# Kernel optimization log

Measured on AMD Instinct MI355X. Metric: run time of the kernel, lower is better.

Reference implementation:

```python
import jax, jax.numpy as jnp
import numpy as np

N, S, IN_F, TEXT_D, EMB, H = 128, 1024, 768, 512, 512, 8
HD = EMB // H  # 64


def setup_inputs() -> dict:
    key = jax.random.key(0)
    ks = jax.random.split(key, 14)
    sc = 0.02
    return {
        "v": jax.random.normal(ks[0], (1, N, 12, IN_F), dtype=jnp.float32),
        "t": jax.random.normal(ks[1], (N, S, TEXT_D), dtype=jnp.float32),
        "t_len": jax.random.randint(ks[2], (N,), 1, S + 1, dtype=jnp.int32),
        "W_fc1": jax.random.normal(ks[3], (EMB, IN_F), dtype=jnp.float32) * sc,
        "b_fc1": jnp.zeros((EMB,), jnp.float32),
        "W_fc2": jax.random.normal(ks[4], (EMB, 12 * EMB), dtype=jnp.float32) * sc,
        "b_fc2": jnp.zeros((EMB,), jnp.float32),
        "Wq": jax.random.normal(ks[5], (EMB, EMB), dtype=jnp.float32) * sc,
        "Wk": jax.random.normal(ks[6], (EMB, TEXT_D), dtype=jnp.float32) * sc,
        "Wv": jax.random.normal(ks[7], (EMB, TEXT_D), dtype=jnp.float32) * sc,
        "bq": jnp.zeros((EMB,), jnp.float32),
        "bk": jnp.zeros((EMB,), jnp.float32),
        "bv": jnp.zeros((EMB,), jnp.float32),
        "Wo": jax.random.normal(ks[8], (EMB, EMB), dtype=jnp.float32) * sc,
        "bo": jnp.zeros((EMB,), jnp.float32),
    }


def reference(v, t, t_len, W_fc1, b_fc1, W_fc2, b_fc2, Wq, Wk, Wv, bq, bk, bv, Wo, bo):
    # fc1 + ReLU: [1,N,12,IN_F] -> [N,12,EMB]
    x = jax.nn.relu(jnp.einsum('onif,ef->onie', v, W_fc1) + b_fc1)[0]
    # flatten + fc2 + ReLU -> [N, EMB]
    x = x.reshape(N, 12 * EMB)
    vfeat = jax.nn.relu(x @ W_fc2.T + b_fc2)
    # Batched ragged multihead attention, query length 1 per item.
    scale = 1.0 / jnp.sqrt(jnp.asarray(HD, vfeat.dtype))
    q = ((vfeat @ Wq.T + bq) * scale).reshape(N, H, HD)           # [N,H,HD]
    k = (jnp.einsum('nsd,ed->nse', t, Wk) + bk).reshape(N, S, H, HD)
    vv = (jnp.einsum('nsd,ed->nse', t, Wv) + bv).reshape(N, S, H, HD)
    scores = jnp.einsum('nhd,nshd->nhs', q, k)                    # [N,H,S]
    valid = (jnp.arange(S)[None, :] < t_len[:, None])[:, None, :]  # [N,1,S]
    scores = jnp.where(valid, scores, jnp.finfo(scores.dtype).min)
    w = jax.nn.softmax(scores, axis=-1)                           # [N,H,S]
    ctx = jnp.einsum('nhs,nshd->nhd', w, vv).reshape(N, EMB)
    attn_out = ctx @ Wo.T + bo                                    # [N,EMB]
    return vfeat, attn_out
```

## Files before the change

### kernel.cpp

```cpp
#include <hip/hip_runtime.h>

#define NB 128
#define SSEQ 1024
#define TD 512
#define NSPLIT 16

typedef _Float16 half8 __attribute__((ext_vector_type(8)));
typedef _Float16 half4 __attribute__((ext_vector_type(4)));
typedef _Float16 half2v __attribute__((ext_vector_type(2)));
typedef float f32x4 __attribute__((ext_vector_type(4)));
typedef float f32x2 __attribute__((ext_vector_type(2)));

__global__ __launch_bounds__(256) void k_cvt(
    const float* __restrict__ v, const float* __restrict__ w1,
    const float* __restrict__ w2, const float* __restrict__ wq,
    const float* __restrict__ wv, const float* __restrict__ wo,
    _Float16* __restrict__ v16, _Float16* __restrict__ w1h,
    _Float16* __restrict__ w2h, _Float16* __restrict__ wqh,
    _Float16* __restrict__ wvh, _Float16* __restrict__ woh)
{
  int i = blockIdx.x * 256 + threadIdx.x;
  const float* src; _Float16* dst; long j;
  if      (i < 294912)  { src = v;  dst = v16; j = i; }
  else if (i < 393216)  { src = w1; dst = w1h; j = i - 294912; }
  else if (i < 1179648) { src = w2; dst = w2h; j = i - 393216; }
  else if (i < 1245184) { src = wq; dst = wqh; j = i - 1179648; }
  else if (i < 1310720) { src = wv; dst = wvh; j = i - 1245184; }
  else if (i < 1376256) { src = wo; dst = woh; j = i - 1310720; }
  else return;
  f32x4 x = *(const f32x4*)(src + 4 * j);
  *(half4*)(dst + 4 * j) = __builtin_convertvector(x, half4);
}

__global__ __launch_bounds__(256) void k_gemm(
    const _Float16* __restrict__ A, int lda, long aSZ,
    const _Float16* __restrict__ B, int ldb, long bSZ,
    const float* __restrict__ bias, float scale, int doRelu, int outMode,
    float* __restrict__ outF, _Float16* __restrict__ outH,
    int ldc, int cColOff, int mtiles, int kTiles, long oSplit)
{
  __shared__ _Float16 As[64][72];
  __shared__ _Float16 Bs[64][72];
  int mt = blockIdx.x % mtiles, nt = blockIdx.x / mtiles;
  int sp = blockIdx.y, bz = blockIdx.z;
  int tid = threadIdx.x;
  int r = tid >> 2, kq = (tid & 3) * 16;
  int w = tid >> 6, l = tid & 63;
  const _Float16* Ab = A + (long)bz * aSZ + (long)(mt * 64) * lda + (long)sp * kTiles * 64;
  const _Float16* Bb = B + (long)bz * bSZ + (long)(nt * 64) * ldb + (long)sp * kTiles * 64;
  const _Float16* ap = Ab + (long)r * lda + kq;
  const _Float16* bp = Bb + (long)r * ldb + kq;
  half8 ag0 = *(const half8*)ap, ag1 = *(const half8*)(ap + 8);
  half8 bg0 = *(const half8*)bp, bg1 = *(const half8*)(bp + 8);
  f32x4 acc[4];
  #pragma unroll
  for (int c = 0; c < 4; ++c) acc[c] = (f32x4){0.f, 0.f, 0.f, 0.f};
  int fr = l & 15, fo = (l >> 4) * 8;
  for (int kt = 0; kt < kTiles; ++kt) {
    __syncthreads();
    *(half8*)&As[r][kq] = ag0; *(half8*)&As[r][kq + 8] = ag1;
    *(half8*)&Bs[r][kq] = bg0; *(half8*)&Bs[r][kq + 8] = bg1;
    __syncthreads();
    if (kt + 1 < kTiles) {
      ap += 64; bp += 64;
      ag0 = *(const half8*)ap; ag1 = *(const half8*)(ap + 8);
      bg0 = *(const half8*)bp; bg1 = *(const half8*)(bp + 8);
    }
    #pragma unroll
    for (int ks = 0; ks < 2; ++ks) {
      half8 af = *(const half8*)&As[16 * w + fr][ks * 32 + fo];
      #pragma unroll
      for (int c = 0; c < 4; ++c) {
        half8 bf = *(const half8*)&Bs[16 * c + fr][ks * 32 + fo];
        acc[c] = __builtin_amdgcn_mfma_f32_16x16x32_f16(af, bf, acc[c], 0, 0, 0);
      }
    }
  }
  int lrow = (l >> 4) * 4, lcol = l & 15;
  #pragma unroll
  for (int c = 0; c < 4; ++c) {
    #pragma unroll
    for (int rr = 0; rr < 4; ++rr) {
      int gm = mt * 64 + 16 * w + lrow + rr;
      int gn = nt * 64 + 16 * c + lcol;
      int ecol = gn + bz * cColOff;
      float vv = acc[c][rr];
      if (bias) vv += bias[ecol];
      vv *= scale;
      if (doRelu) vv = fmaxf(vv, 0.f);
      long oidx = (long)gm * ldc + ecol;
      if (outMode == 0) outF[oidx] = vv;
      else if (outMode == 1) outH[oidx] = (_Float16)vv;
      else outF[oidx + (long)sp * oSplit] = vv;
    }
  }
}

__global__ __launch_bounds__(256) void k_vfeat(
    const float* __restrict__ vacc, const float* __restrict__ b2,
    float* __restrict__ outF, _Float16* __restrict__ vf16)
{
  int i = blockIdx.x * 256 + threadIdx.x;
  float vv = b2[i & 511];
  #pragma unroll
  for (int sp = 0; sp < 16; ++sp) vv += vacc[sp * 65536 + i];
  vv = fmaxf(vv, 0.f);
  outF[i] = vv;
  vf16[i] = (_Float16)vv;
}

__global__ __launch_bounds__(256) void k_qk(
    const float* __restrict__ qacc, const float* __restrict__ bq,
    const float* __restrict__ Wk, const float* __restrict__ bk,
    _Float16* __restrict__ qk16, float* __restrict__ qb)
{
  int n = blockIdx.x, tid = threadIdx.x;
  __shared__ float qs[512];
  #pragma unroll
  for (int o = 0; o < 2; ++o) {
    int d = tid + o * 256;
    float q0 = qacc[n * 512 + d] + qacc[65536 + n * 512 + d]
             + qacc[131072 + n * 512 + d] + qacc[196608 + n * 512 + d];
    qs[d] = (q0 + bq[d]) * 0.125f;
  }
  __syncthreads();
  _Float16* qn = qk16 + (long)n * 8192;
  #pragma unroll 1
  for (int h = 0; h < 8; ++h) {
    float a0 = 0.f, a1 = 0.f;
    #pragma unroll 8
    for (int j = 0; j < 64; ++j) {
      float qv = qs[h * 64 + j];
      const float* wr = Wk + (long)(h * 64 + j) * 512;
      a0 = fmaf(qv, wr[tid], a0);
      a1 = fmaf(qv, wr[tid + 256], a1);
    }
    qn[h * 512 + tid] = (_Float16)a0;
    qn[h * 512 + tid + 256] = (_Float16)a1;
  }
  #pragma unroll
  for (int h = 8; h < 16; ++h) {
    qn[h * 512 + tid] = (_Float16)0.f;
    qn[h * 512 + tid + 256] = (_Float16)0.f;
  }
  if (tid < 64) {
    #pragma unroll 1
    for (int h = 0; h < 8; ++h) {
      float pb = qs[h * 64 + tid] * bk[h * 64 + tid];
      #pragma unroll
      for (int m = 1; m < 64; m <<= 1) pb += __shfl_xor(pb, m, 64);
      if (tid == 0) qb[n * 8 + h] = pb;
    }
  }
}

__global__ __launch_bounds__(256, 4) void k_attn(
    const float* __restrict__ t, const int* __restrict__ tlen,
    const _Float16* __restrict__ qk16, const float* __restrict__ qb,
    float* __restrict__ pu, float* __restrict__ pl)
{
  int n = blockIdx.x >> 4, sp = blockIdx.x & 15;
  int len = tlen[n];
  int chunk = (len + NSPLIT - 1) / NSPLIT;
  int s0 = sp * chunk;
  int s1 = s0 + chunk; if (s1 > len) s1 = len;
  if (s0 >= s1) return;
  int tid = threadIdx.x, wid = tid >> 6, l = tid & 63;

  __shared__ __align__(16) _Float16 ts[32][520];
  __shared__ __align__(16) float ws[32][8];
  __shared__ float lred[8];

  const _Float16* qn = qk16 + (long)n * 8192;
  int fr = l & 15, fo = (l >> 4) * 8;
  half8 qfrag[16];
  #pragma unroll
  for (int kt = 0; kt < 16; ++kt)
    qfrag[kt] = *(const half8*)(qn + fr * 512 + kt * 32 + fo);
  float qbr = (fr < 8) ? qb[n * 8 + fr] : 0.f;

  f32x2 u[8];
  #pragma unroll
  for (int h = 0; h < 8; ++h) u[h] = (f32x2){0.f, 0.f};
  float lac = 0.f;
  if (tid < 8) lred[tid] = 0.f;

  const float* tn = t + (long)n * SSEQ * TD;
  int col0 = 128 * wid + 2 * l;

  for (int base = s0; base < s1; base += 32) {
    __syncthreads();
    {
      f32x4 a0, a1, b0, b1;
      auto ld = [&](int c, f32x4& x0, f32x4& x1) {
        int sg = base + c * 4 + wid;
        if (sg < s1) {
          const float* p = tn + (long)sg * TD;
          x0 = *(const f32x4*)(p + 4 * l);
          x1 = *(const f32x4*)(p + 256 + 4 * l);
        } else {
          x0 = (f32x4){0.f,0.f,0.f,0.f}; x1 = (f32x4){0.f,0.f,0.f,0.f};
        }
      };
      ld(0, a0, a1); ld(1, b0, b1);
      #pragma unroll
      for (int c = 0; c < 8; c += 2) {
        half4 h0 = __builtin_convertvector(a0, half4);
        half4 h1 = __builtin_convertvector(a1, half4);
        int row = c * 4 + wid;
        if (c + 2 < 8) ld(c + 2, a0, a1);
        *(half4*)&ts[row][4 * l] = h0;
        *(half4*)&ts[row][256 + 4 * l] = h1;
        half4 g0 = __builtin_convertvector(b0, half4);
        half4 g1 = __builtin_convertvector(b1, half4);
        int row2 = c * 4 + 4 + wid;
        if (c + 3 < 8) ld(c + 3, b0, b1);
        *(half4*)&ts[row2][4 * l] = g0;
        *(half4*)&ts[row2][256 + 4 * l] = g1;
      }
    }
    __syncthreads();
    if (wid < 2) {
      f32x4 acc = (f32x4){0.f, 0.f, 0.f, 0.f};
      #pragma unroll
      for (int kt = 0; kt < 16; ++kt) {
        half8 af = *(const half8*)&ts[16 * wid + fr][kt * 32 + fo];
        acc = __builtin_amdgcn_mfma_f32_16x16x32_f16(af, qfrag[kt], acc, 0, 0, 0);
      }
      #pragma unroll
      for (int r = 0; r < 4; ++r) {
        int sl = 16 * wid + (l >> 4) * 4 + r;
        float wv = 0.f;
        if (fr < 8 && base + sl < s1) wv = __expf(acc[r] + qbr);
        if (fr < 8) ws[sl][fr] = wv;
        lac += wv;
      }
    }
    __syncthreads();
    #pragma unroll 4
    for (int r = 0; r < 32; ++r) {
      f32x4 wa = *(const f32x4*)&ws[r][0];
      f32x4 wb = *(const f32x4*)&ws[r][4];
      half2v tv = *(const half2v*)&ts[r][col0];
      f32x2 tp = { (float)tv[0], (float)tv[1] };
      u[0] += wa[0] * tp; u[1] += wa[1] * tp;
      u[2] += wa[2] * tp; u[3] += wa[3] * tp;
      u[4] += wb[0] * tp; u[5] += wb[1] * tp;
      u[6] += wb[2] * tp; u[7] += wb[3] * tp;
    }
  }
  float* pn = pu + (long)n * 4096;
  #pragma unroll
  for (int h = 0; h < 8; ++h) {
    atomicAdd(&pn[h * 512 + col0], u[h][0]);
    atomicAdd(&pn[h * 512 + col0 + 1], u[h][1]);
  }
  if (wid < 2 && fr < 8) atomicAdd(&lred[fr], lac);
  __syncthreads();
  if (tid < 8) atomicAdd(&pl[n * 8 + tid], lred[tid]);
}

__global__ __launch_bounds__(256) void k_norm(
    const float* __restrict__ pu, const float* __restrict__ pl,
    _Float16* __restrict__ un16)
{
  int n = blockIdx.x, tid = threadIdx.x;
  __shared__ float linv[8];
  if (tid < 8) linv[tid] = 1.f / pl[n * 8 + tid];
  __syncthreads();
  for (int i = tid; i < 4096; i += 256) {
    int h = i >> 9, d = i & 511;
    float sacc = pu[(long)n * 4096 + i];
    un16[(long)h * 65536 + n * 512 + d] = (_Float16)(sacc * linv[h]);
  }
}

extern "C" void kernel_launch(void* const* d_in, const int* in_sizes, int n_in,
                              void* d_out, int out_size, void* d_ws, size_t ws_size,
                              hipStream_t stream)
{
  const float* t    = (const float*)d_in[1];
  const int*   tlen = (const int*)d_in[2];
  const float* b1   = (const float*)d_in[4];
  const float* b2   = (const float*)d_in[6];
  const float* Wk   = (const float*)d_in[8];
  const float* bq   = (const float*)d_in[10];
  const float* bk   = (const float*)d_in[11];
  const float* bv   = (const float*)d_in[12];
  const float* bo   = (const float*)d_in[14];
  float* out = (float*)d_out;

  _Float16* hb   = (_Float16*)d_ws;
  _Float16* v16  = hb;
  _Float16* w1h  = hb + 1179648l;
  _Float16* w2h  = hb + 1572864l;
  _Float16* wqh  = hb + 4718592l;
  _Float16* wvh  = hb + 4980736l;
  _Float16* woh  = hb + 5242880l;
  _Float16* x16  = hb + 5505024l;
  _Float16* vf16 = hb + 6291456l;
  _Float16* ctx16= hb + 6356992l;
  _Float16* un16 = hb + 6422528l;
  _Float16* qk16 = hb + 6946816l;
  float* fb   = (float*)(hb + 7995392l);
  float* vacc = fb;
  float* qacc = fb + 1048576l;
  float* qb   = fb + 1310720l;
  float* pu   = fb + 1311744l;
  float* pl   = fb + 1836032l;

  hipMemsetAsync(pu, 0, (524288l + 1024l) * sizeof(float), stream);
  k_cvt<<<5376, 256, 0, stream>>>((const float*)d_in[0], (const float*)d_in[3],
                                  (const float*)d_in[5], (const float*)d_in[7],
                                  (const float*)d_in[9], (const float*)d_in[13],
                                  v16, w1h, w2h, wqh, wvh, woh);
  k_gemm<<<dim3(192, 1, 1), 256, 0, stream>>>(v16, 768, 0, w1h, 768, 0,
      b1, 1.f, 1, 1, nullptr, x16, 512, 0, 24, 12, 0);
  k_gemm<<<dim3(16, 16, 1), 256, 0, stream>>>(x16, 6144, 0, w2h, 6144, 0,
      nullptr, 1.f, 0, 2, vacc, nullptr, 512, 0, 2, 6, 65536);
  k_vfeat<<<256, 256, 0, stream>>>(vacc, b2, out, vf16);
  k_gemm<<<dim3(16, 4, 1), 256, 0, stream>>>(vf16, 512, 0, wqh, 512, 0,
      nullptr, 1.f, 0, 2, qacc, nullptr, 512, 0, 2, 2, 65536);
  k_qk<<<128, 256, 0, stream>>>(qacc, bq, Wk, bk, qk16, qb);
  k_attn<<<NB * NSPLIT, 256, 0, stream>>>(t, tlen, qk16, qb, pu, pl);
  k_norm<<<128, 256, 0, stream>>>(pu, pl, un16);
  k_gemm<<<dim3(2, 1, 8), 256, 0, stream>>>(un16, 512, 65536, wvh, 512, 32768,
      bv, 1.f, 0, 1, nullptr, ctx16, 512, 64, 2, 8, 0);
  k_gemm<<<dim3(16, 1, 1), 256, 0, stream>>>(ctx16, 512, 0, woh, 512, 0,
      bo, 1.f, 0, 0, out + 65536, nullptr, 512, 0, 2, 8, 0);
}
```

Measured before the change: 480.3 us.

## Fuse fp32-to-fp16 conversion into GEMMs, drop norm kernel, split attention per 32-row tile

```diff
diff --git a/kernel.cpp b/kernel.cpp
--- a/kernel.cpp
+++ b/kernel.cpp
@@ -3,7 +3,6 @@
 #define NB 128
 #define SSEQ 1024
 #define TD 512
-#define NSPLIT 16
 
 typedef _Float16 half8 __attribute__((ext_vector_type(8)));
 typedef _Float16 half4 __attribute__((ext_vector_type(4)));
@@ -11,31 +10,12 @@
 typedef float f32x4 __attribute__((ext_vector_type(4)));
 typedef float f32x2 __attribute__((ext_vector_type(2)));
 
-__global__ __launch_bounds__(256) void k_cvt(
-    const float* __restrict__ v, const float* __restrict__ w1,
-    const float* __restrict__ w2, const float* __restrict__ wq,
-    const float* __restrict__ wv, const float* __restrict__ wo,
-    _Float16* __restrict__ v16, _Float16* __restrict__ w1h,
-    _Float16* __restrict__ w2h, _Float16* __restrict__ wqh,
-    _Float16* __restrict__ wvh, _Float16* __restrict__ woh)
-{
-  int i = blockIdx.x * 256 + threadIdx.x;
-  const float* src; _Float16* dst; long j;
-  if      (i < 294912)  { src = v;  dst = v16; j = i; }
-  else if (i < 393216)  { src = w1; dst = w1h; j = i - 294912; }
-  else if (i < 1179648) { src = w2; dst = w2h; j = i - 393216; }
-  else if (i < 1245184) { src = wq; dst = wqh; j = i - 1179648; }
-  else if (i < 1310720) { src = wv; dst = wvh; j = i - 1245184; }
-  else if (i < 1376256) { src = wo; dst = woh; j = i - 1310720; }
-  else return;
-  f32x4 x = *(const f32x4*)(src + 4 * j);
-  *(half4*)(dst + 4 * j) = __builtin_convertvector(x, half4);
-}
-
+template<int AM, int BM>
 __global__ __launch_bounds__(256) void k_gemm(
-    const _Float16* __restrict__ A, int lda, long aSZ,
-    const _Float16* __restrict__ B, int ldb, long bSZ,
-    const float* __restrict__ bias, float scale, int doRelu, int outMode,
+    const void* __restrict__ Av, int lda, long aSZ,
+    const void* __restrict__ Bv, int ldb, long bSZ,
+    const float* __restrict__ bias, const float* __restrict__ aRowScale,
+    float scale, int doRelu, int outMode,
     float* __restrict__ outF, _Float16* __restrict__ outH,
     int ldc, int cColOff, int mtiles, int kTiles, long oSplit)
 {
@@ -46,25 +26,57 @@
   int tid = threadIdx.x;
   int r = tid >> 2, kq = (tid & 3) * 16;
   int w = tid >> 6, l = tid & 63;
-  const _Float16* Ab = A + (long)bz * aSZ + (long)(mt * 64) * lda + (long)sp * kTiles * 64;
-  const _Float16* Bb = B + (long)bz * bSZ + (long)(nt * 64) * ldb + (long)sp * kTiles * 64;
-  const _Float16* ap = Ab + (long)r * lda + kq;
-  const _Float16* bp = Bb + (long)r * ldb + kq;
-  half8 ag0 = *(const half8*)ap, ag1 = *(const half8*)(ap + 8);
-  half8 bg0 = *(const half8*)bp, bg1 = *(const half8*)(bp + 8);
+  long aoff = (long)bz * aSZ + (long)(mt * 64 + r) * lda + (long)sp * kTiles * 64 + kq;
+  long boff = (long)bz * bSZ + (long)(nt * 64 + r) * ldb + (long)sp * kTiles * 64 + kq;
+  const _Float16* apH = (const _Float16*)Av + aoff;
+  const float*    apF = (const float*)Av + aoff;
+  const _Float16* bpH = (const _Float16*)Bv + boff;
+  const float*    bpF = (const float*)Bv + boff;
+  float srA = 1.0f;
+  if constexpr (AM == 2) srA = 1.0f / aRowScale[(mt * 64 + r) * 8 + bz];
+
+  half8 pa0, pa1, pb0, pb1;
+  f32x4 qa0, qa1, qa2, qa3, qc0, qc1, qc2, qc3;
+  if constexpr (AM == 0) { pa0 = *(const half8*)apH; pa1 = *(const half8*)(apH + 8); }
+  else { qa0 = *(const f32x4*)apF; qa1 = *(const f32x4*)(apF + 4);
+         qa2 = *(const f32x4*)(apF + 8); qa3 = *(const f32x4*)(apF + 12); }
+  if constexpr (BM == 0) { pb0 = *(const half8*)bpH; pb1 = *(const half8*)(bpH + 8); }
+  else { qc0 = *(const f32x4*)bpF; qc1 = *(const f32x4*)(bpF + 4);
+         qc2 = *(const f32x4*)(bpF + 8); qc3 = *(const f32x4*)(bpF + 12); }
+
   f32x4 acc[4];
   #pragma unroll
   for (int c = 0; c < 4; ++c) acc[c] = (f32x4){0.f, 0.f, 0.f, 0.f};
   int fr = l & 15, fo = (l >> 4) * 8;
   for (int kt = 0; kt < kTiles; ++kt) {
     __syncthreads();
-    *(half8*)&As[r][kq] = ag0; *(half8*)&As[r][kq + 8] = ag1;
-    *(half8*)&Bs[r][kq] = bg0; *(half8*)&Bs[r][kq + 8] = bg1;
+    if constexpr (AM == 0) {
+      *(half8*)&As[r][kq] = pa0; *(half8*)&As[r][kq + 8] = pa1;
+    } else {
+      f32x4 s0 = qa0, s1 = qa1, s2 = qa2, s3 = qa3;
+      if constexpr (AM == 2) { s0 *= srA; s1 *= srA; s2 *= srA; s3 *= srA; }
+      *(half4*)&As[r][kq + 0]  = __builtin_convertvector(s0, half4);
+      *(half4*)&As[r][kq + 4]  = __builtin_convertvector(s1, half4);
+      *(half4*)&As[r][kq + 8]  = __builtin_convertvector(s2, half4);
+      *(half4*)&As[r][kq + 12] = __builtin_convertvector(s3, half4);
+    }
+    if constexpr (BM == 0) {
+      *(half8*)&Bs[r][kq] = pb0; *(half8*)&Bs[r][kq + 8] = pb1;
+    } else {
+      *(half4*)&Bs[r][kq + 0]  = __builtin_convertvector(qc0, half4);
+      *(half4*)&Bs[r][kq + 4]  = __builtin_convertvector(qc1, half4);
+      *(half4*)&Bs[r][kq + 8]  = __builtin_convertvector(qc2, half4);
+      *(half4*)&Bs[r][kq + 12] = __builtin_convertvector(qc3, half4);
+    }
     __syncthreads();
     if (kt + 1 < kTiles) {
-      ap += 64; bp += 64;
-      ag0 = *(const half8*)ap; ag1 = *(const half8*)(ap + 8);
-      bg0 = *(const half8*)bp; bg1 = *(const half8*)(bp + 8);
+      apH += 64; apF += 64; bpH += 64; bpF += 64;
+      if constexpr (AM == 0) { pa0 = *(const half8*)apH; pa1 = *(const half8*)(apH + 8); }
+      else { qa0 = *(const f32x4*)apF; qa1 = *(const f32x4*)(apF + 4);
+             qa2 = *(const f32x4*)(apF + 8); qa3 = *(const f32x4*)(apF + 12); }
+      if constexpr (BM == 0) { pb0 = *(const half8*)bpH; pb1 = *(const half8*)(bpH + 8); }
+      else { qc0 = *(const f32x4*)bpF; qc1 = *(const f32x4*)(bpF + 4);
+             qc2 = *(const f32x4*)(bpF + 8); qc3 = *(const f32x4*)(bpF + 12); }
     }
     #pragma unroll
     for (int ks = 0; ks < 2; ++ks) {
@@ -110,19 +122,13 @@
 }
 
 __global__ __launch_bounds__(256) void k_qk(
-    const float* __restrict__ qacc, const float* __restrict__ bq,
-    const float* __restrict__ Wk, const float* __restrict__ bk,
-    _Float16* __restrict__ qk16, float* __restrict__ qb)
+    const float* __restrict__ qf, const float* __restrict__ Wk,
+    const float* __restrict__ bk, _Float16* __restrict__ qk16, float* __restrict__ qb)
 {
   int n = blockIdx.x, tid = threadIdx.x;
   __shared__ float qs[512];
-  #pragma unroll
-  for (int o = 0; o < 2; ++o) {
-    int d = tid + o * 256;
-    float q0 = qacc[n * 512 + d] + qacc[65536 + n * 512 + d]
-             + qacc[131072 + n * 512 + d] + qacc[196608 + n * 512 + d];
-    qs[d] = (q0 + bq[d]) * 0.125f;
-  }
+  qs[tid] = qf[n * 512 + tid];
+  qs[tid + 256] = qf[n * 512 + tid + 256];
   __syncthreads();
   _Float16* qn = qk16 + (long)n * 8192;
   #pragma unroll 1
@@ -154,100 +160,91 @@
   }
 }
 
-__global__ __launch_bounds__(256, 4) void k_attn(
+__global__ __launch_bounds__(256) void k_attn(
     const float* __restrict__ t, const int* __restrict__ tlen,
     const _Float16* __restrict__ qk16, const float* __restrict__ qb,
     float* __restrict__ pu, float* __restrict__ pl)
 {
-  int n = blockIdx.x >> 4, sp = blockIdx.x & 15;
+  int n = blockIdx.x >> 5, j = blockIdx.x & 31;
   int len = tlen[n];
-  int chunk = (len + NSPLIT - 1) / NSPLIT;
-  int s0 = sp * chunk;
-  int s1 = s0 + chunk; if (s1 > len) s1 = len;
-  if (s0 >= s1) return;
+  int base = j * 32;
+  if (base >= len) return;
+  int s1 = base + 32; if (s1 > len) s1 = len;
   int tid = threadIdx.x, wid = tid >> 6, l = tid & 63;
 
   __shared__ __align__(16) _Float16 ts[32][520];
   __shared__ __align__(16) float ws[32][8];
   __shared__ float lred[8];
-
-  const _Float16* qn = qk16 + (long)n * 8192;
+  if (tid < 8) lred[tid] = 0.f;
+
+  const float* tn = t + (long)n * SSEQ * TD;
+  {
+    f32x4 a0, a1, b0, b1;
+    auto ld = [&](int c, f32x4& x0, f32x4& x1) {
+      int sg = base + c * 4 + wid;
+      if (sg < s1) {
+        const float* p = tn + (long)sg * TD;
+        x0 = *(const f32x4*)(p + 4 * l);
+        x1 = *(const f32x4*)(p + 256 + 4 * l);
+      } else {
+        x0 = (f32x4){0.f,0.f,0.f,0.f}; x1 = (f32x4){0.f,0.f,0.f,0.f};
+      }
+    };
+    ld(0, a0, a1); ld(1, b0, b1);
+    #pragma unroll
+    for (int c = 0; c < 8; c += 2) {
+      half4 h0 = __builtin_convertvector(a0, half4);
+      half4 h1 = __builtin_convertvector(a1, half4);
+      int row = c * 4 + wid;
+      if (c + 2 < 8) ld(c + 2, a0, a1);
+      *(half4*)&ts[row][4 * l] = h0;
+      *(half4*)&ts[row][256 + 4 * l] = h1;
+      half4 g0 = __builtin_convertvector(b0, half4);
+      half4 g1 = __builtin_convertvector(b1, half4);
+      int row2 = c * 4 + 4 + wid;
+      if (c + 3 < 8) ld(c + 3, b0, b1);
+      *(half4*)&ts[row2][4 * l] = g0;
+      *(half4*)&ts[row2][256 + 4 * l] = g1;
+    }
+  }
+  __syncthreads();
   int fr = l & 15, fo = (l >> 4) * 8;
-  half8 qfrag[16];
-  #pragma unroll
-  for (int kt = 0; kt < 16; ++kt)
-    qfrag[kt] = *(const half8*)(qn + fr * 512 + kt * 32 + fo);
-  float qbr = (fr < 8) ? qb[n * 8 + fr] : 0.f;
-
+  if (wid < 2) {
+    const _Float16* qn = qk16 + (long)n * 8192 + fr * 512 + fo;
+    f32x4 acc = (f32x4){0.f, 0.f, 0.f, 0.f};
+    #pragma unroll 4
+    for (int kt = 0; kt < 16; ++kt) {
+      half8 bf = *(const half8*)(qn + kt * 32);
+      half8 af = *(const half8*)&ts[16 * wid + fr][kt * 32 + fo];
+      acc = __builtin_amdgcn_mfma_f32_16x16x32_f16(af, bf, acc, 0, 0, 0);
+    }
+    float qbr = (fr < 8) ? qb[n * 8 + fr] : 0.f;
+    float lac = 0.f;
+    #pragma unroll
+    for (int r = 0; r < 4; ++r) {
+      int sl = 16 * wid + (l >> 4) * 4 + r;
+      float wv = 0.f;
+      if (fr < 8 && base + sl < s1) wv = __expf(acc[r] + qbr);
+      if (fr < 8) ws[sl][fr] = wv;
+      lac += wv;
+    }
+    if (fr < 8) atomicAdd(&lred[fr], lac);
+  }
+  __syncthreads();
+  int col0 = 128 * wid + 2 * l;
   f32x2 u[8];
   #pragma unroll
   for (int h = 0; h < 8; ++h) u[h] = (f32x2){0.f, 0.f};
-  float lac = 0.f;
-  if (tid < 8) lred[tid] = 0.f;
-
-  const float* tn = t + (long)n * SSEQ * TD;
-  int col0 = 128 * wid + 2 * l;
-
-  for (int base = s0; base < s1; base += 32) {
-    __syncthreads();
-    {
-      f32x4 a0, a1, b0, b1;
-      auto ld = [&](int c, f32x4& x0, f32x4& x1) {
-        int sg = base + c * 4 + wid;
-        if (sg < s1) {
-          const float* p = tn + (long)sg * TD;
-          x0 = *(const f32x4*)(p + 4 * l);
-          x1 = *(const f32x4*)(p + 256 + 4 * l);
-        } else {
-          x0 = (f32x4){0.f,0.f,0.f,0.f}; x1 = (f32x4){0.f,0.f,0.f,0.f};
-        }
-      };
-      ld(0, a0, a1); ld(1, b0, b1);
-      #pragma unroll
-      for (int c = 0; c < 8; c += 2) {
-        half4 h0 = __builtin_convertvector(a0, half4);
-        half4 h1 = __builtin_convertvector(a1, half4);
-        int row = c * 4 + wid;
-        if (c + 2 < 8) ld(c + 2, a0, a1);
-        *(half4*)&ts[row][4 * l] = h0;
-        *(half4*)&ts[row][256 + 4 * l] = h1;
-        half4 g0 = __builtin_convertvector(b0, half4);
-        half4 g1 = __builtin_convertvector(b1, half4);
-        int row2 = c * 4 + 4 + wid;
-        if (c + 3 < 8) ld(c + 3, b0, b1);
-        *(half4*)&ts[row2][4 * l] = g0;
-        *(half4*)&ts[row2][256 + 4 * l] = g1;
-      }
-    }
-    __syncthreads();
-    if (wid < 2) {
-      f32x4 acc = (f32x4){0.f, 0.f, 0.f, 0.f};
-      #pragma unroll
-      for (int kt = 0; kt < 16; ++kt) {
-        half8 af = *(const half8*)&ts[16 * wid + fr][kt * 32 + fo];
-        acc = __builtin_amdgcn_mfma_f32_16x16x32_f16(af, qfrag[kt], acc, 0, 0, 0);
-      }
-      #pragma unroll
-      for (int r = 0; r < 4; ++r) {
-        int sl = 16 * wid + (l >> 4) * 4 + r;
-        float wv = 0.f;
-        if (fr < 8 && base + sl < s1) wv = __expf(acc[r] + qbr);
-        if (fr < 8) ws[sl][fr] = wv;
-        lac += wv;
-      }
-    }
-    __syncthreads();
-    #pragma unroll 4
-    for (int r = 0; r < 32; ++r) {
-      f32x4 wa = *(const f32x4*)&ws[r][0];
-      f32x4 wb = *(const f32x4*)&ws[r][4];
-      half2v tv = *(const half2v*)&ts[r][col0];
-      f32x2 tp = { (float)tv[0], (float)tv[1] };
-      u[0] += wa[0] * tp; u[1] += wa[1] * tp;
-      u[2] += wa[2] * tp; u[3] += wa[3] * tp;
-      u[4] += wb[0] * tp; u[5] += wb[1] * tp;
-      u[6] += wb[2] * tp; u[7] += wb[3] * tp;
-    }
+  #pragma unroll 4
+  for (int r = 0; r < 32; ++r) {
+    f32x4 wa = *(const f32x4*)&ws[r][0];
+    f32x4 wb = *(const f32x4*)&ws[r][4];
+    half2v tv = *(const half2v*)&ts[r][col0];
+    f32x2 tp = { (float)tv[0], (float)tv[1] };
+    u[0] += wa[0] * tp; u[1] += wa[1] * tp;
+    u[2] += wa[2] * tp; u[3] += wa[3] * tp;
+    u[4] += wb[0] * tp; u[5] += wb[1] * tp;
+    u[6] += wb[2] * tp; u[7] += wb[3] * tp;
   }
   float* pn = pu + (long)n * 4096;
   #pragma unroll
@@ -255,77 +252,54 @@
     atomicAdd(&pn[h * 512 + col0], u[h][0]);
     atomicAdd(&pn[h * 512 + col0 + 1], u[h][1]);
   }
-  if (wid < 2 && fr < 8) atomicAdd(&lred[fr], lac);
-  __syncthreads();
   if (tid < 8) atomicAdd(&pl[n * 8 + tid], lred[tid]);
-}
-
-__global__ __launch_bounds__(256) void k_norm(
-    const float* __restrict__ pu, const float* __restrict__ pl,
-    _Float16* __restrict__ un16)
-{
-  int n = blockIdx.x, tid = threadIdx.x;
-  __shared__ float linv[8];
-  if (tid < 8) linv[tid] = 1.f / pl[n * 8 + tid];
-  __syncthreads();
-  for (int i = tid; i < 4096; i += 256) {
-    int h = i >> 9, d = i & 511;
-    float sacc = pu[(long)n * 4096 + i];
-    un16[(long)h * 65536 + n * 512 + d] = (_Float16)(sacc * linv[h]);
-  }
 }
 
 extern "C" void kernel_launch(void* const* d_in, const int* in_sizes, int n_in,
                               void* d_out, int out_size, void* d_ws, size_t ws_size,
                               hipStream_t stream)
 {
+  const float* v    = (const float*)d_in[0];
   const float* t    = (const float*)d_in[1];
   const int*   tlen = (const int*)d_in[2];
+  const float* W1   = (const float*)d_in[3];
   const float* b1   = (const float*)d_in[4];
+  const float* W2   = (const float*)d_in[5];
   const float* b2   = (const float*)d_in[6];
+  const float* Wq   = (const float*)d_in[7];
   const float* Wk   = (const float*)d_in[8];
+  const float* Wv   = (const float*)d_in[9];
   const float* bq   = (const float*)d_in[10];
   const float* bk   = (const float*)d_in[11];
   const float* bv   = (const float*)d_in[12];
+  const float* Wo   = (const float*)d_in[13];
   const float* bo   = (const float*)d_in[14];
   float* out = (float*)d_out;
 
   _Float16* hb   = (_Float16*)d_ws;
-  _Float16* v16  = hb;
-  _Float16* w1h  = hb + 1179648l;
-  _Float16* w2h  = hb + 1572864l;
-  _Float16* wqh  = hb + 4718592l;
-  _Float16* wvh  = hb + 4980736l;
-  _Float16* woh  = hb + 5242880l;
-  _Float16* x16  = hb + 5505024l;
-  _Float16* vf16 = hb + 6291456l;
-  _Float16* ctx16= hb + 6356992l;
-  _Float16* un16 = hb + 6422528l;
-  _Float16* qk16 = hb + 6946816l;
-  float* fb   = (float*)(hb + 7995392l);
+  _Float16* x16  = hb;
+  _Float16* vf16 = hb + 786432l;
+  _Float16* ctx16= hb + 851968l;
+  _Float16* qk16 = hb + 917504l;
+  float* fb   = (float*)(hb + 1966080l);
   float* vacc = fb;
-  float* qacc = fb + 1048576l;
-  float* qb   = fb + 1310720l;
-  float* pu   = fb + 1311744l;
-  float* pl   = fb + 1836032l;
+  float* qf   = fb + 1048576l;
+  float* pu   = fb + 1114112l;
+  float* pl   = fb + 1638400l;
+  float* qb   = fb + 1639424l;
 
   hipMemsetAsync(pu, 0, (524288l + 1024l) * sizeof(float), stream);
-  k_cvt<<<5376, 256, 0, stream>>>((const float*)d_in[0], (const float*)d_in[3],
-                                  (const float*)d_in[5], (const float*)d_in[7],
-                                  (const float*)d_in[9], (const float*)d_in[13],
-                                  v16, w1h, w2h, wqh, wvh, woh);
-  k_gemm<<<dim3(192, 1, 1), 256, 0, stream>>>(v16, 768, 0, w1h, 768, 0,
-      b1, 1.f, 1, 1, nullptr, x16, 512, 0, 24, 12, 0);
-  k_gemm<<<dim3(16, 16, 1), 256, 0, stream>>>(x16, 6144, 0, w2h, 6144, 0,
-      nullptr, 1.f, 0, 2, vacc, nullptr, 512, 0, 2, 6, 65536);
+  k_gemm<1,1><<<dim3(192, 1, 1), 256, 0, stream>>>(v, 768, 0, W1, 768, 0,
+      b1, nullptr, 1.f, 1, 1, nullptr, x16, 512, 0, 24, 12, 0);
+  k_gemm<0,1><<<dim3(16, 16, 1), 256, 0, stream>>>(x16, 6144, 0, W2, 6144, 0,
+      nullptr, nullptr, 1.f, 0, 2, vacc, nullptr, 512, 0, 2, 6, 65536);
   k_vfeat<<<256, 256, 0, stream>>>(vacc, b2, out, vf16);
-  k_gemm<<<dim3(16, 4, 1), 256, 0, stream>>>(vf16, 512, 0, wqh, 512, 0,
-      nullptr, 1.f, 0, 2, qacc, nullptr, 512, 0, 2, 2, 65536);
-  k_qk<<<128, 256, 0, stream>>>(qacc, bq, Wk, bk, qk16, qb);
-  k_attn<<<NB * NSPLIT, 256, 0, stream>>>(t, tlen, qk16, qb, pu, pl);
-  k_norm<<<128, 256, 0, stream>>>(pu, pl, un16);
-  k_gemm<<<dim3(2, 1, 8), 256, 0, stream>>>(un16, 512, 65536, wvh, 512, 32768,
-      bv, 1.f, 0, 1, nullptr, ctx16, 512, 64, 2, 8, 0);
-  k_gemm<<<dim3(16, 1, 1), 256, 0, stream>>>(ctx16, 512, 0, woh, 512, 0,
-      bo, 1.f, 0, 0, out + 65536, nullptr, 512, 0, 2, 8, 0);
-}
+  k_gemm<0,1><<<dim3(16, 1, 1), 256, 0, stream>>>(vf16, 512, 0, Wq, 512, 0,
+      bq, nullptr, 0.125f, 0, 0, qf, nullptr, 512, 0, 2, 8, 0);
+  k_qk<<<128, 256, 0, stream>>>(qf, Wk, bk, qk16, qb);
+  k_attn<<<NB * 32, 256, 0, stream>>>(t, tlen, qk16, qb, pu, pl);
+  k_gemm<2,1><<<dim3(2, 1, 8), 256, 0, stream>>>(pu, 4096, 512, Wv, 512, 32768,
+      bv, pl, 1.f, 0, 1, nullptr, ctx16, 512, 64, 2, 8, 0);
+  k_gemm<0,1><<<dim3(16, 1, 1), 256, 0, stream>>>(ctx16, 512, 0, Wo, 512, 0,
+      bo, nullptr, 1.f, 0, 0, out + 65536, nullptr, 512, 0, 2, 8, 0);
+}
```

Result: slower. 518.9 us (+8.0%).
